# Kernel tuning notes

Measured on AMD Instinct MI355X. Metric: run time of the kernel, lower is better.

## Reference

```python
import jax, jax.numpy as jnp
import numpy as np

NUM_RANGES = 256
DOPPLER = 64
EMBED = 16
MAX_ELE = 37
MAX_AZI = 107
K_PER_RANGE = 512
IN_DIM = DOPPLER + 2 * EMBED  # 96


def setup_inputs() -> dict:
    key = jax.random.key(0)
    ks = jax.random.split(key, 12)
    N = NUM_RANGES * K_PER_RANGE
    s = 1.0 / np.sqrt(IN_DIM)  # torch Linear default init scale
    return {
        "power_vals": jax.random.normal(ks[0], (N, DOPPLER), dtype=jnp.float32),
        "ele_indices": jax.random.randint(ks[1], (N,), 0, MAX_ELE, dtype=jnp.int32),
        "range_indices": jax.random.randint(ks[2], (N,), 0, NUM_RANGES, dtype=jnp.int32),
        "azi_indices": jax.random.randint(ks[3], (N,), 0, MAX_AZI, dtype=jnp.int32),
        "ele_table": jax.random.normal(ks[4], (MAX_ELE, EMBED), dtype=jnp.float32),
        "azi_table": jax.random.normal(ks[5], (MAX_AZI, EMBED), dtype=jnp.float32),
        "Wq": jax.random.uniform(ks[6], (DOPPLER, IN_DIM), jnp.float32, -s, s),
        "bq": jax.random.uniform(ks[7], (DOPPLER,), jnp.float32, -s, s),
        "Wk": jax.random.uniform(ks[8], (DOPPLER, IN_DIM), jnp.float32, -s, s),
        "bk": jax.random.uniform(ks[9], (DOPPLER,), jnp.float32, -s, s),
        "Wv": jax.random.uniform(ks[10], (DOPPLER, IN_DIM), jnp.float32, -s, s),
        "bv": jax.random.uniform(ks[11], (DOPPLER,), jnp.float32, -s, s),
    }


def reference(power_vals, ele_indices, range_indices, azi_indices,
              ele_table, azi_table, Wq, bq, Wk, bk, Wv, bv):
    Kp = power_vals.shape[0] // NUM_RANGES
    # embedding gather + concat: [R, K, D + 2E]
    ele_e = ele_table[ele_indices.reshape(NUM_RANGES, Kp)]
    azi_e = azi_table[azi_indices.reshape(NUM_RANGES, Kp)]
    pv = power_vals.reshape(NUM_RANGES, Kp, DOPPLER)
    x = jnp.concatenate([pv, ele_e, azi_e], axis=-1)
    # QKV projections (torch Linear: x @ W.T + b)
    Q = jnp.einsum('rkf,df->rkd', x, Wq) + bq
    Kt = jnp.einsum('rkf,df->rkd', x, Wk) + bk
    V = jnp.einsum('rkf,df->rkd', x, Wv) + bv
    scores = jnp.einsum('rqd,rkd->rqk', Q, Kt) / jnp.sqrt(jnp.float32(DOPPLER))
    attn = jax.nn.softmax(scores, axis=-1)
    attended = jnp.einsum('rqk,rkd->rqd', attn, V)
    attended_sum = attended.sum(axis=-1)  # [R, K]
    return attended_sum.reshape(-1)
```

## Files before the change

kernel.cpp:

```cpp
#include <hip/hip_runtime.h>


#define SCALE 0.18033688011112042f

typedef __bf16 bf16;
typedef bf16 v4bf __attribute__((ext_vector_type(4)));
typedef bf16 v8bf __attribute__((ext_vector_type(8)));
typedef float v4f __attribute__((ext_vector_type(4)));

__device__ __forceinline__ v8bf pk8(float4 a, float4 b) {
    v8bf r;
    r[0] = (bf16)a.x; r[1] = (bf16)a.y; r[2] = (bf16)a.z; r[3] = (bf16)a.w;
    r[4] = (bf16)b.x; r[5] = (bf16)b.y; r[6] = (bf16)b.z; r[7] = (bf16)b.w;
    return r;
}
__device__ __forceinline__ float d4(float4 a, v4f w) {
    return a.x * w[0] + a.y * w[1] + a.z * w[2] + a.w * w[3];
}

__global__ __launch_bounds__(1024, 4)
void sda_kernel(const float* __restrict__ power,
                const int*   __restrict__ ele_i,
                const int*   __restrict__ azi_i,
                const float* __restrict__ ele_t,
                const float* __restrict__ azi_t,
                const float* __restrict__ Wq, const float* __restrict__ bq,
                const float* __restrict__ Wk, const float* __restrict__ bk,
                const float* __restrict__ Wv, const float* __restrict__ bv,
                float* __restrict__ out)
{
    extern __shared__ char smem[];
    char*  Kb   = smem;
    float* vsum = (float*)(smem + 65536);
    float* wvs  = (float*)(smem + 67584);
    bf16*  WqL  = (bf16*)(smem + 68096);
    bf16*  WkL  = (bf16*)(smem + 80384);
    float* bqL  = (float*)(smem + 92672);
    float* bkL  = (float*)(smem + 92928);
    int*   flags= (int*)(smem + 93184);
    float* pbuf = (float*)smem;

    const int tid  = threadIdx.x;
    const int wave = tid >> 6;
    const int lane = tid & 63;
    const int l15  = lane & 15;
    const int quad = lane >> 4;
    const int rowbase = blockIdx.x * 512 + wave * 32;

#pragma unroll
    for (int i = 0; i < 6; i++) {
        int idx = tid + i * 1024;
        WqL[idx] = (bf16)Wq[idx];
        WkL[idx] = (bf16)Wk[idx];
    }
    if (tid < 768) {
        int c = tid % 96;
        int g = tid / 96;
        float s = 0.f;
#pragma unroll
        for (int r = 0; r < 8; r++) s += Wv[(g * 8 + r) * 96 + c];
        pbuf[g * 96 + c] = s;
    } else if (tid < 832) {
        pbuf[768 + (tid - 768)] = bv[tid - 768];
    }
    if (tid < 64) { bqL[tid] = bq[tid]; bkL[tid] = bk[tid]; }
    if (tid >= 832 && tid < 848) flags[tid - 832] = 0;
    __syncthreads();
    if (tid < 96) {
        float s = 0.f;
#pragma unroll
        for (int g = 0; g < 8; g++) s += pbuf[g * 96 + tid];
        wvs[tid] = s;
    } else if (tid == 96) {
        float s = 0.f;
#pragma unroll
        for (int j = 0; j < 64; j++) s += pbuf[768 + j];
        wvs[96] = s;
    }
    __syncthreads();

    v8bf xa[2][3];
#pragma unroll
    for (int mt = 0; mt < 2; mt++) {
        int row = rowbase + mt * 16 + l15;
        const float* pr = power + (size_t)row * 64;
        float d;
        {
            float4 a0 = *(const float4*)(pr + quad * 8);
            float4 a1 = *(const float4*)(pr + quad * 8 + 4);
            xa[mt][0] = pk8(a0, a1);
            d  = d4(a0, *(const v4f*)(wvs + quad * 8))
               + d4(a1, *(const v4f*)(wvs + quad * 8 + 4));
        }
        {
            float4 a2 = *(const float4*)(pr + 32 + quad * 8);
            float4 a3 = *(const float4*)(pr + 32 + quad * 8 + 4);
            xa[mt][1] = pk8(a2, a3);
            d += d4(a2, *(const v4f*)(wvs + 32 + quad * 8))
               + d4(a3, *(const v4f*)(wvs + 32 + quad * 8 + 4));
        }
        {
            int ie = ele_i[row];
            int ia = azi_i[row];
            const float* tb = (quad < 2) ? (ele_t + ie * 16 + quad * 8)
                                         : (azi_t + ia * 16 + (quad - 2) * 8);
            float4 a4 = *(const float4*)tb;
            float4 a5 = *(const float4*)(tb + 4);
            xa[mt][2] = pk8(a4, a5);
            d += d4(a4, *(const v4f*)(wvs + 64 + quad * 8))
               + d4(a5, *(const v4f*)(wvs + 64 + quad * 8 + 4));
        }
        d += __shfl_xor(d, 16);
        d += __shfl_xor(d, 32);
        if (quad == 0) vsum[wave * 32 + mt * 16 + l15] = d + wvs[96];
    }

    char* Sw = Kb + wave * 4096;
#pragma unroll 1
    for (int mtd = 0; mtd < 4; mtd++) {
        const bf16* wrow = WqL + (mtd * 16 + l15) * 96;
        v8bf wq3[3];
#pragma unroll
        for (int kt = 0; kt < 3; kt++)
            wq3[kt] = *(const v8bf*)(wrow + kt * 32 + quad * 8);
        float4 bq4 = *(const float4*)(bqL + mtd * 16 + quad * 4);
#pragma unroll
        for (int ntr = 0; ntr < 2; ntr++) {
            v4f acc = {0.f, 0.f, 0.f, 0.f};
#pragma unroll
            for (int kt = 0; kt < 3; kt++)
                acc = __builtin_amdgcn_mfma_f32_16x16x32_bf16(wq3[kt], xa[ntr][kt], acc, 0, 0, 0);
            int row = ntr * 16 + l15;
            v4bf o;
            o[0] = (bf16)((acc[0] + bq4.x) * SCALE);
            o[1] = (bf16)((acc[1] + bq4.y) * SCALE);
            o[2] = (bf16)((acc[2] + bq4.z) * SCALE);
            o[3] = (bf16)((acc[3] + bq4.w) * SCALE);
            *(v4bf*)(Sw + row * 128 +
                     ((((mtd * 2 + (quad >> 1)) ^ (row & 7)) << 4) | ((quad & 1) << 3))) = o;
        }
    }
    v8bf qf[2][2];
#pragma unroll
    for (int nt = 0; nt < 2; nt++)
#pragma unroll
        for (int kt = 0; kt < 2; kt++)
            qf[nt][kt] = *(const v8bf*)(Sw + (nt * 16 + l15) * 128 +
                                        (((kt * 4 + quad) ^ (l15 & 7)) << 4));

#pragma unroll 1
    for (int mtd = 0; mtd < 4; mtd++) {
        const bf16* wrow = WkL + (mtd * 16 + l15) * 96;
        v8bf wk3[3];
#pragma unroll
        for (int kt = 0; kt < 3; kt++)
            wk3[kt] = *(const v8bf*)(wrow + kt * 32 + quad * 8);
        float4 bk4 = *(const float4*)(bkL + mtd * 16 + quad * 4);
#pragma unroll
        for (int ntr = 0; ntr < 2; ntr++) {
            v4f acc = {0.f, 0.f, 0.f, 0.f};
#pragma unroll
            for (int kt = 0; kt < 3; kt++)
                acc = __builtin_amdgcn_mfma_f32_16x16x32_bf16(wk3[kt], xa[ntr][kt], acc, 0, 0, 0);
            int keyb = wave * 32 + ntr * 16 + l15;
            v4bf o;
            o[0] = (bf16)(acc[0] + bk4.x);
            o[1] = (bf16)(acc[1] + bk4.y);
            o[2] = (bf16)(acc[2] + bk4.z);
            o[3] = (bf16)(acc[3] + bk4.w);
            *(v4bf*)(Kb + keyb * 128 +
                     ((((mtd * 2 + (quad >> 1)) ^ (keyb & 7)) << 4) | ((quad & 1) << 3))) = o;
        }
    }
    if (lane == 0) ((volatile int*)flags)[wave] = 1;

    float osum[2] = {0.f, 0.f};
    float lsum[2] = {0.f, 0.f};
#pragma unroll 1
    for (int t = 0; t < 16; t++) {
        while (((volatile int*)flags)[t] == 0) {}
        asm volatile("" ::: "memory");
        v8bf kf[2][2];
#pragma unroll
        for (int mtk = 0; mtk < 2; mtk++)
#pragma unroll
            for (int kt = 0; kt < 2; kt++) {
                int key = t * 32 + mtk * 16 + l15;
                kf[mtk][kt] = *(const v8bf*)(Kb + key * 128 + (((kt * 4 + quad) ^ (key & 7)) << 4));
            }
        v4f vs[2];
#pragma unroll
        for (int mtk = 0; mtk < 2; mtk++)
            vs[mtk] = *(const v4f*)(vsum + t * 32 + mtk * 16 + quad * 4);
#pragma unroll
        for (int mtk = 0; mtk < 2; mtk++) {
#pragma unroll
            for (int nt = 0; nt < 2; nt++) {
                v4f acc = {0.f, 0.f, 0.f, 0.f};
                acc = __builtin_amdgcn_mfma_f32_16x16x32_bf16(kf[mtk][0], qf[nt][0], acc, 0, 0, 0);
                acc = __builtin_amdgcn_mfma_f32_16x16x32_bf16(kf[mtk][1], qf[nt][1], acc, 0, 0, 0);
                float p0 = __builtin_amdgcn_exp2f(acc[0]);
                float p1 = __builtin_amdgcn_exp2f(acc[1]);
                float p2 = __builtin_amdgcn_exp2f(acc[2]);
                float p3 = __builtin_amdgcn_exp2f(acc[3]);
                lsum[nt] += (p0 + p1) + (p2 + p3);
                osum[nt] += ((p0 * vs[mtk][0] + p1 * vs[mtk][1]) +
                             (p2 * vs[mtk][2] + p3 * vs[mtk][3]));
            }
        }
    }

#pragma unroll
    for (int nt = 0; nt < 2; nt++) {
        float lv = lsum[nt];
        lv += __shfl_xor(lv, 16);
        lv += __shfl_xor(lv, 32);
        float ov = osum[nt];
        ov += __shfl_xor(ov, 16);
        ov += __shfl_xor(ov, 32);
        if (quad == 0) out[rowbase + nt * 16 + l15] = ov / lv;
    }
}

extern "C" void kernel_launch(void* const* d_in, const int* in_sizes, int n_in,
                              void* d_out, int out_size, void* d_ws, size_t ws_size,
                              hipStream_t stream) {
    const float* power = (const float*)d_in[0];
    const int*   ele_i = (const int*)d_in[1];
    const int*   azi_i = (const int*)d_in[3];
    const float* ele_t = (const float*)d_in[4];
    const float* azi_t = (const float*)d_in[5];
    const float* Wq = (const float*)d_in[6];
    const float* bq = (const float*)d_in[7];
    const float* Wk = (const float*)d_in[8];
    const float* bk = (const float*)d_in[9];
    const float* Wv = (const float*)d_in[10];
    const float* bv = (const float*)d_in[11];
    float* out = (float*)d_out;

    const int lds_bytes = 93248;
    (void)hipFuncSetAttribute(reinterpret_cast<const void*>(sda_kernel),
                              hipFuncAttributeMaxDynamicSharedMemorySize, lds_bytes);
    sda_kernel<<<256, 1024, lds_bytes, stream>>>(power, ele_i, azi_i, ele_t, azi_t,
                                                 Wq, bq, Wk, bk, Wv, bv, out);
}
```

Baseline: 111.5 us.

## Split waves into producer projection and consumer attention roles with flag handoff

Half of the 16 waves now load inputs and compute the Q and K projections for 64 rows each, publishing Q and K tiles to LDS behind per-tile flags. The other 8 waves spin (with s_sleep) on those flags and run the attention loop over 64 queries each, reusing each K fragment across four query tiles. The aim is to overlap the projection phase with attention and to improve K reuse per wave. In exchange, LDS use rises to about 155 KB, which still fits one 1024-thread block per CU. The consumer waves are also idle until their Q tiles are ready, so attention runs on only half the waves.

```diff
diff --git a/kernel.cpp b/kernel.cpp
--- a/kernel.cpp
+++ b/kernel.cpp
@@ -30,22 +30,24 @@
                 float* __restrict__ out)
 {
     extern __shared__ char smem[];
-    char*  Kb   = smem;
-    float* vsum = (float*)(smem + 65536);
-    float* wvs  = (float*)(smem + 67584);
-    bf16*  WqL  = (bf16*)(smem + 68096);
-    bf16*  WkL  = (bf16*)(smem + 80384);
-    float* bqL  = (float*)(smem + 92672);
-    float* bkL  = (float*)(smem + 92928);
-    int*   flags= (int*)(smem + 93184);
-    float* pbuf = (float*)smem;
+    char*  Kb    = smem;
+    char*  Qb    = smem + 65536;
+    float* vsum  = (float*)(smem + 131072);
+    float* wvs   = (float*)(smem + 133120);
+    bf16*  WqL   = (bf16*)(smem + 133632);
+    bf16*  WkL   = (bf16*)(smem + 145920);
+    float* bqL   = (float*)(smem + 158208);
+    float* bkL   = (float*)(smem + 158464);
+    int*   kflag = (int*)(smem + 158720);
+    int*   qflag = (int*)(smem + 158784);
+    float* pbuf  = (float*)smem;
 
     const int tid  = threadIdx.x;
     const int wave = tid >> 6;
     const int lane = tid & 63;
     const int l15  = lane & 15;
     const int quad = lane >> 4;
-    const int rowbase = blockIdx.x * 512 + wave * 32;
+    const int range = blockIdx.x;
 
 #pragma unroll
     for (int i = 0; i < 6; i++) {
@@ -64,7 +66,7 @@
         pbuf[768 + (tid - 768)] = bv[tid - 768];
     }
     if (tid < 64) { bqL[tid] = bq[tid]; bkL[tid] = bk[tid]; }
-    if (tid >= 832 && tid < 848) flags[tid - 832] = 0;
+    if (tid >= 832 && tid < 856) kflag[tid - 832] = 0;
     __syncthreads();
     if (tid < 96) {
         float s = 0.f;
@@ -79,146 +81,161 @@
     }
     __syncthreads();
 
-    v8bf xa[2][3];
-#pragma unroll
-    for (int mt = 0; mt < 2; mt++) {
-        int row = rowbase + mt * 16 + l15;
-        const float* pr = power + (size_t)row * 64;
-        float d;
-        {
-            float4 a0 = *(const float4*)(pr + quad * 8);
-            float4 a1 = *(const float4*)(pr + quad * 8 + 4);
-            xa[mt][0] = pk8(a0, a1);
-            d  = d4(a0, *(const v4f*)(wvs + quad * 8))
-               + d4(a1, *(const v4f*)(wvs + quad * 8 + 4));
-        }
-        {
-            float4 a2 = *(const float4*)(pr + 32 + quad * 8);
-            float4 a3 = *(const float4*)(pr + 32 + quad * 8 + 4);
-            xa[mt][1] = pk8(a2, a3);
-            d += d4(a2, *(const v4f*)(wvs + 32 + quad * 8))
-               + d4(a3, *(const v4f*)(wvs + 32 + quad * 8 + 4));
-        }
-        {
-            int ie = ele_i[row];
-            int ia = azi_i[row];
-            const float* tb = (quad < 2) ? (ele_t + ie * 16 + quad * 8)
-                                         : (azi_t + ia * 16 + (quad - 2) * 8);
-            float4 a4 = *(const float4*)tb;
-            float4 a5 = *(const float4*)(tb + 4);
-            xa[mt][2] = pk8(a4, a5);
-            d += d4(a4, *(const v4f*)(wvs + 64 + quad * 8))
-               + d4(a5, *(const v4f*)(wvs + 64 + quad * 8 + 4));
-        }
-        d += __shfl_xor(d, 16);
-        d += __shfl_xor(d, 32);
-        if (quad == 0) vsum[wave * 32 + mt * 16 + l15] = d + wvs[96];
-    }
-
-    char* Sw = Kb + wave * 4096;
-#pragma unroll 1
-    for (int mtd = 0; mtd < 4; mtd++) {
-        const bf16* wrow = WqL + (mtd * 16 + l15) * 96;
-        v8bf wq3[3];
-#pragma unroll
-        for (int kt = 0; kt < 3; kt++)
-            wq3[kt] = *(const v8bf*)(wrow + kt * 32 + quad * 8);
-        float4 bq4 = *(const float4*)(bqL + mtd * 16 + quad * 4);
-#pragma unroll
-        for (int ntr = 0; ntr < 2; ntr++) {
-            v4f acc = {0.f, 0.f, 0.f, 0.f};
+    if (wave >= 8) {
+        const int b = wave - 8;
+        const int rowbase = range * 512 + b * 64;
+
+        v8bf xa[4][3];
+#pragma unroll
+        for (int mt = 0; mt < 4; mt++) {
+            int row = rowbase + mt * 16 + l15;
+            const float* pr = power + (size_t)row * 64;
+            float d;
+            {
+                float4 a0 = *(const float4*)(pr + quad * 8);
+                float4 a1 = *(const float4*)(pr + quad * 8 + 4);
+                xa[mt][0] = pk8(a0, a1);
+                d  = d4(a0, *(const v4f*)(wvs + quad * 8))
+                   + d4(a1, *(const v4f*)(wvs + quad * 8 + 4));
+            }
+            {
+                float4 a2 = *(const float4*)(pr + 32 + quad * 8);
+                float4 a3 = *(const float4*)(pr + 32 + quad * 8 + 4);
+                xa[mt][1] = pk8(a2, a3);
+                d += d4(a2, *(const v4f*)(wvs + 32 + quad * 8))
+                   + d4(a3, *(const v4f*)(wvs + 32 + quad * 8 + 4));
+            }
+            {
+                int ie = ele_i[row];
+                int ia = azi_i[row];
+                const float* tb = (quad < 2) ? (ele_t + ie * 16 + quad * 8)
+                                             : (azi_t + ia * 16 + (quad - 2) * 8);
+                float4 a4 = *(const float4*)tb;
+                float4 a5 = *(const float4*)(tb + 4);
+                xa[mt][2] = pk8(a4, a5);
+                d += d4(a4, *(const v4f*)(wvs + 64 + quad * 8))
+                   + d4(a5, *(const v4f*)(wvs + 64 + quad * 8 + 4));
+            }
+            d += __shfl_xor(d, 16);
+            d += __shfl_xor(d, 32);
+            if (quad == 0) vsum[b * 64 + mt * 16 + l15] = d + wvs[96];
+        }
+
+#pragma unroll 1
+        for (int mtd = 0; mtd < 4; mtd++) {
+            const bf16* wrow = WqL + (mtd * 16 + l15) * 96;
+            v8bf wq3[3];
 #pragma unroll
             for (int kt = 0; kt < 3; kt++)
-                acc = __builtin_amdgcn_mfma_f32_16x16x32_bf16(wq3[kt], xa[ntr][kt], acc, 0, 0, 0);
-            int row = ntr * 16 + l15;
-            v4bf o;
-            o[0] = (bf16)((acc[0] + bq4.x) * SCALE);
-            o[1] = (bf16)((acc[1] + bq4.y) * SCALE);
-            o[2] = (bf16)((acc[2] + bq4.z) * SCALE);
-            o[3] = (bf16)((acc[3] + bq4.w) * SCALE);
-            *(v4bf*)(Sw + row * 128 +
-                     ((((mtd * 2 + (quad >> 1)) ^ (row & 7)) << 4) | ((quad & 1) << 3))) = o;
-        }
-    }
-    v8bf qf[2][2];
-#pragma unroll
-    for (int nt = 0; nt < 2; nt++)
-#pragma unroll
-        for (int kt = 0; kt < 2; kt++)
-            qf[nt][kt] = *(const v8bf*)(Sw + (nt * 16 + l15) * 128 +
-                                        (((kt * 4 + quad) ^ (l15 & 7)) << 4));
-
-#pragma unroll 1
-    for (int mtd = 0; mtd < 4; mtd++) {
-        const bf16* wrow = WkL + (mtd * 16 + l15) * 96;
-        v8bf wk3[3];
-#pragma unroll
-        for (int kt = 0; kt < 3; kt++)
-            wk3[kt] = *(const v8bf*)(wrow + kt * 32 + quad * 8);
-        float4 bk4 = *(const float4*)(bkL + mtd * 16 + quad * 4);
-#pragma unroll
-        for (int ntr = 0; ntr < 2; ntr++) {
-            v4f acc = {0.f, 0.f, 0.f, 0.f};
-#pragma unroll
-            for (int kt = 0; kt < 3; kt++)
-                acc = __builtin_amdgcn_mfma_f32_16x16x32_bf16(wk3[kt], xa[ntr][kt], acc, 0, 0, 0);
-            int keyb = wave * 32 + ntr * 16 + l15;
-            v4bf o;
-            o[0] = (bf16)(acc[0] + bk4.x);
-            o[1] = (bf16)(acc[1] + bk4.y);
-            o[2] = (bf16)(acc[2] + bk4.z);
-            o[3] = (bf16)(acc[3] + bk4.w);
-            *(v4bf*)(Kb + keyb * 128 +
-                     ((((mtd * 2 + (quad >> 1)) ^ (keyb & 7)) << 4) | ((quad & 1) << 3))) = o;
-        }
-    }
-    if (lane == 0) ((volatile int*)flags)[wave] = 1;
-
-    float osum[2] = {0.f, 0.f};
-    float lsum[2] = {0.f, 0.f};
-#pragma unroll 1
-    for (int t = 0; t < 16; t++) {
-        while (((volatile int*)flags)[t] == 0) {}
+                wq3[kt] = *(const v8bf*)(wrow + kt * 32 + quad * 8);
+            float4 bq4 = *(const float4*)(bqL + mtd * 16 + quad * 4);
+#pragma unroll
+            for (int ntr = 0; ntr < 4; ntr++) {
+                v4f acc = {0.f, 0.f, 0.f, 0.f};
+#pragma unroll
+                for (int kt = 0; kt < 3; kt++)
+                    acc = __builtin_amdgcn_mfma_f32_16x16x32_bf16(wq3[kt], xa[ntr][kt], acc, 0, 0, 0);
+                int q = b * 64 + ntr * 16 + l15;
+                v4bf o;
+                o[0] = (bf16)((acc[0] + bq4.x) * SCALE);
+                o[1] = (bf16)((acc[1] + bq4.y) * SCALE);
+                o[2] = (bf16)((acc[2] + bq4.z) * SCALE);
+                o[3] = (bf16)((acc[3] + bq4.w) * SCALE);
+                *(v4bf*)(Qb + q * 128 +
+                         ((((mtd * 2 + (quad >> 1)) ^ (q & 7)) << 4) | ((quad & 1) << 3))) = o;
+            }
+        }
+        if (lane == 0) ((volatile int*)qflag)[b] = 1;
+
+#pragma unroll 1
+        for (int half = 0; half < 2; half++) {
+#pragma unroll 1
+            for (int mtd = 0; mtd < 4; mtd++) {
+                const bf16* wrow = WkL + (mtd * 16 + l15) * 96;
+                v8bf wk3[3];
+#pragma unroll
+                for (int kt = 0; kt < 3; kt++)
+                    wk3[kt] = *(const v8bf*)(wrow + kt * 32 + quad * 8);
+                float4 bk4 = *(const float4*)(bkL + mtd * 16 + quad * 4);
+#pragma unroll
+                for (int n2 = 0; n2 < 2; n2++) {
+                    v4f acc = {0.f, 0.f, 0.f, 0.f};
+#pragma unroll
+                    for (int kt = 0; kt < 3; kt++)
+                        acc = __builtin_amdgcn_mfma_f32_16x16x32_bf16(wk3[kt], xa[half * 2 + n2][kt], acc, 0, 0, 0);
+                    int keyb = b * 64 + half * 32 + n2 * 16 + l15;
+                    v4bf o;
+                    o[0] = (bf16)(acc[0] + bk4.x);
+                    o[1] = (bf16)(acc[1] + bk4.y);
+                    o[2] = (bf16)(acc[2] + bk4.z);
+                    o[3] = (bf16)(acc[3] + bk4.w);
+                    *(v4bf*)(Kb + keyb * 128 +
+                             ((((mtd * 2 + (quad >> 1)) ^ (keyb & 7)) << 4) | ((quad & 1) << 3))) = o;
+                }
+            }
+            if (lane == 0) ((volatile int*)kflag)[2 * b + half] = 1;
+        }
+    } else {
+        const int a = wave;
+
+        while (((volatile int*)qflag)[a] == 0) __builtin_amdgcn_s_sleep(1);
         asm volatile("" ::: "memory");
-        v8bf kf[2][2];
-#pragma unroll
-        for (int mtk = 0; mtk < 2; mtk++)
-#pragma unroll
-            for (int kt = 0; kt < 2; kt++) {
-                int key = t * 32 + mtk * 16 + l15;
-                kf[mtk][kt] = *(const v8bf*)(Kb + key * 128 + (((kt * 4 + quad) ^ (key & 7)) << 4));
-            }
-        v4f vs[2];
-#pragma unroll
-        for (int mtk = 0; mtk < 2; mtk++)
-            vs[mtk] = *(const v4f*)(vsum + t * 32 + mtk * 16 + quad * 4);
-#pragma unroll
-        for (int mtk = 0; mtk < 2; mtk++) {
-#pragma unroll
-            for (int nt = 0; nt < 2; nt++) {
-                v4f acc = {0.f, 0.f, 0.f, 0.f};
-                acc = __builtin_amdgcn_mfma_f32_16x16x32_bf16(kf[mtk][0], qf[nt][0], acc, 0, 0, 0);
-                acc = __builtin_amdgcn_mfma_f32_16x16x32_bf16(kf[mtk][1], qf[nt][1], acc, 0, 0, 0);
-                float p0 = __builtin_amdgcn_exp2f(acc[0]);
-                float p1 = __builtin_amdgcn_exp2f(acc[1]);
-                float p2 = __builtin_amdgcn_exp2f(acc[2]);
-                float p3 = __builtin_amdgcn_exp2f(acc[3]);
-                lsum[nt] += (p0 + p1) + (p2 + p3);
-                osum[nt] += ((p0 * vs[mtk][0] + p1 * vs[mtk][1]) +
-                             (p2 * vs[mtk][2] + p3 * vs[mtk][3]));
-            }
-        }
-    }
-
-#pragma unroll
-    for (int nt = 0; nt < 2; nt++) {
-        float lv = lsum[nt];
-        lv += __shfl_xor(lv, 16);
-        lv += __shfl_xor(lv, 32);
-        float ov = osum[nt];
-        ov += __shfl_xor(ov, 16);
-        ov += __shfl_xor(ov, 32);
-        if (quad == 0) out[rowbase + nt * 16 + l15] = ov / lv;
+        v8bf qf[4][2];
+#pragma unroll
+        for (int nt = 0; nt < 4; nt++) {
+            int q = a * 64 + nt * 16 + l15;
+#pragma unroll
+            for (int kt = 0; kt < 2; kt++)
+                qf[nt][kt] = *(const v8bf*)(Qb + q * 128 + (((kt * 4 + quad) ^ (q & 7)) << 4));
+        }
+
+        float osum[4] = {0.f, 0.f, 0.f, 0.f};
+        float lsum[4] = {0.f, 0.f, 0.f, 0.f};
+#pragma unroll 1
+        for (int i = 0; i < 16; i++) {
+            int t = (i < 8) ? 2 * i : 2 * (i - 8) + 1;
+            while (((volatile int*)kflag)[t] == 0) __builtin_amdgcn_s_sleep(1);
+            asm volatile("" ::: "memory");
+            v8bf kf[2][2];
+#pragma unroll
+            for (int mtk = 0; mtk < 2; mtk++)
+#pragma unroll
+                for (int kt = 0; kt < 2; kt++) {
+                    int key = t * 32 + mtk * 16 + l15;
+                    kf[mtk][kt] = *(const v8bf*)(Kb + key * 128 + (((kt * 4 + quad) ^ (key & 7)) << 4));
+                }
+            v4f vs[2];
+#pragma unroll
+            for (int mtk = 0; mtk < 2; mtk++)
+                vs[mtk] = *(const v4f*)(vsum + t * 32 + mtk * 16 + quad * 4);
+#pragma unroll
+            for (int mtk = 0; mtk < 2; mtk++) {
+#pragma unroll
+                for (int qg = 0; qg < 4; qg++) {
+                    v4f acc = {0.f, 0.f, 0.f, 0.f};
+                    acc = __builtin_amdgcn_mfma_f32_16x16x32_bf16(kf[mtk][0], qf[qg][0], acc, 0, 0, 0);
+                    acc = __builtin_amdgcn_mfma_f32_16x16x32_bf16(kf[mtk][1], qf[qg][1], acc, 0, 0, 0);
+                    float p0 = __builtin_amdgcn_exp2f(acc[0]);
+                    float p1 = __builtin_amdgcn_exp2f(acc[1]);
+                    float p2 = __builtin_amdgcn_exp2f(acc[2]);
+                    float p3 = __builtin_amdgcn_exp2f(acc[3]);
+                    lsum[qg] += (p0 + p1) + (p2 + p3);
+                    osum[qg] += ((p0 * vs[mtk][0] + p1 * vs[mtk][1]) +
+                                 (p2 * vs[mtk][2] + p3 * vs[mtk][3]));
+                }
+            }
+        }
+
+#pragma unroll
+        for (int qg = 0; qg < 4; qg++) {
+            float lv = lsum[qg];
+            lv += __shfl_xor(lv, 16);
+            lv += __shfl_xor(lv, 32);
+            float ov = osum[qg];
+            ov += __shfl_xor(ov, 16);
+            ov += __shfl_xor(ov, 32);
+            if (quad == 0) out[range * 512 + a * 64 + qg * 16 + l15] = ov / lv;
+        }
     }
 }
 
@@ -238,7 +255,7 @@
     const float* bv = (const float*)d_in[11];
     float* out = (float*)d_out;
 
-    const int lds_bytes = 93248;
+    const int lds_bytes = 158848;
     (void)hipFuncSetAttribute(reinterpret_cast<const void*>(sda_kernel),
                               hipFuncAttributeMaxDynamicSharedMemorySize, lds_bytes);
     sda_kernel<<<256, 1024, lds_bytes, stream>>>(power, ele_i, azi_i, ele_t, azi_t,
```

After: 121.8 us. 9.2% more time.
